# Kernel tuning notes

Hardware: AMD Instinct MI355X
Metric: run time of the kernel (lower is better)

## Reference

```python
import jax, jax.numpy as jnp
import numpy as np

B, S, D, H = 2, 2048, 1024, 16
HD = D // H  # 64


def setup_inputs() -> dict:
    key = jax.random.key(0)
    k1, k2, k3, k4, k5, k6 = jax.random.split(key, 6)
    x = jax.random.normal(k1, (B, S, D), dtype=jnp.float32)
    # binary mask source (1.0 = masked-out position), multiplied by -1e9 inside
    mask = (jax.random.uniform(k2, (B, S, S), dtype=jnp.float32) < 0.1).astype(jnp.float32)
    lim = 1.0 / np.sqrt(D)
    Wqkv = jax.random.uniform(k3, (D, 3 * D), dtype=jnp.float32, minval=-lim, maxval=lim)
    bqkv = jax.random.uniform(k4, (3 * D,), dtype=jnp.float32, minval=-lim, maxval=lim)
    Wo = jax.random.uniform(k5, (D, D), dtype=jnp.float32, minval=-lim, maxval=lim)
    bo = jax.random.uniform(k6, (D,), dtype=jnp.float32, minval=-lim, maxval=lim)
    return {"x": x, "mask": mask, "Wqkv": Wqkv, "bqkv": bqkv, "Wo": Wo, "bo": bo}


def reference(x, mask, Wqkv, bqkv, Wo, bo):
    b, s, d = x.shape
    qkv = x @ Wqkv + bqkv                              # [B,S,3D]
    qkv = qkv.reshape(b, s, 3, H, HD).transpose(2, 0, 3, 1, 4)  # [3,B,H,S,HD]
    q, k, v = qkv[0], qkv[1], qkv[2]
    scale = 1.0 / jnp.sqrt(jnp.float32(HD))
    scores = jnp.einsum('bhqd,bhkd->bhqk', q, k) * scale
    scores = scores + mask[:, None, :, :] * (-1e9)     # broadcast over heads
    attn = jax.nn.softmax(scores, axis=-1)             # [B,H,S,S]
    values = jnp.einsum('bhqk,bhkd->bhqd', attn, v)    # [B,H,S,HD]
    # faithful to source: permute(1,0,2,3) then reshape(B,S,H*HD)
    values = values.transpose(1, 0, 2, 3).reshape(b, s, H * HD)
    return values @ Wo + bo
```

## Files before the change

kernel.cpp:

```cpp
#include <hip/hip_runtime.h>
#include <stdint.h>

#define BB 2
#define SS 2048
#define DD 1024
#define HH 16
#define HD 64
#define BH 32
#define BS 4096

typedef short bf16x8 __attribute__((ext_vector_type(8)));
typedef float f32x4 __attribute__((ext_vector_type(4)));

static __device__ __forceinline__ unsigned short f2bf(float f) {
    union { float f; unsigned int u; } x;
    x.f = f;
    unsigned int u = x.u;
    unsigned int r = u + 0x7FFFu + ((u >> 16) & 1u);
    return (unsigned short)(r >> 16);
}

static __device__ __forceinline__ void gld16(unsigned short* lds, const unsigned short* g) {
    __builtin_amdgcn_global_load_lds(
        (const __attribute__((address_space(1))) unsigned int*)g,
        (__attribute__((address_space(3))) unsigned int*)lds,
        16, 0, 0);
}

__global__ __launch_bounds__(256) void prep(
    const float* __restrict__ x, unsigned short* __restrict__ xb,
    const float* __restrict__ Wqkv, unsigned short* __restrict__ WqkvT,
    const float* __restrict__ Wo, unsigned short* __restrict__ WoT,
    const float* __restrict__ mask, unsigned int* __restrict__ mbitsT,
    unsigned int* __restrict__ kmaxsq) {
    __shared__ float tile[32][33];
    int bid = blockIdx.x;
    int tid = threadIdx.x;
    if (bid < 4096) {
        int i = (bid * 256 + tid) * 4;
        float4 v = *(const float4*)(x + i);
        ushort4 o;
        o.x = f2bf(v.x); o.y = f2bf(v.y); o.z = f2bf(v.z); o.w = f2bf(v.w);
        *(ushort4*)(xb + i) = o;
    } else if (bid < 8192) {
        const float* W;
        unsigned short* WT;
        int N, t;
        if (bid < 7168) { W = Wqkv; WT = WqkvT; N = 3072; t = bid - 4096; }
        else            { W = Wo;   WT = WoT;   N = 1024; t = bid - 7168; }
        const int K = 1024;
        int nx = N >> 5;
        int n0 = (t % nx) * 32, k0 = (t / nx) * 32;
        int tx = tid & 31, ty = tid >> 5;
#pragma unroll
        for (int i = 0; i < 4; i++)
            tile[ty + i * 8][tx] = W[(size_t)(k0 + ty + i * 8) * N + n0 + tx];
        __syncthreads();
#pragma unroll
        for (int i = 0; i < 4; i++)
            WT[(size_t)(n0 + ty + i * 8) * K + k0 + tx] = f2bf(tile[tx][ty + i * 8]);
    } else if (bid == 8192) {
        if (tid < BH) kmaxsq[tid] = 0u;
    } else {
        size_t i = (size_t)(bid - 8193) * 256 + tid;
        float v = mask[i];
        unsigned long long bal = __ballot(v != 0.0f);
        int lane = tid & 63;
        int kw = (int)((i & 2047) >> 5);
        int sq = (int)((i >> 11) & 2047);
        int b = (int)(i >> 22);
        if (lane == 0)
            mbitsT[((size_t)b * 64 + kw) * 2048 + sq] = (unsigned int)bal;
        else if (lane == 32)
            mbitsT[((size_t)b * 64 + kw) * 2048 + sq] = (unsigned int)(bal >> 32);
    }
}

__global__ __launch_bounds__(256) void k_norm_max(
    const unsigned short* __restrict__ k_ws, unsigned int* __restrict__ kmaxsq) {
    int bh = blockIdx.x >> 3, part = blockIdx.x & 7;
    int row = part * 256 + threadIdx.x;
    const unsigned short* rp = k_ws + ((size_t)bh * 2048 + row) * 64;
    float ss = 0.f;
#pragma unroll
    for (int i = 0; i < 64; i += 8) {
        bf16x8 v;
        __builtin_memcpy(&v, rp + i, 16);
#pragma unroll
        for (int j = 0; j < 8; j++) {
            float f = __uint_as_float(((unsigned int)(unsigned short)v[j]) << 16);
            ss += f * f;
        }
    }
#pragma unroll
    for (int d = 1; d < 64; d <<= 1) ss = fmaxf(ss, __shfl_xor(ss, d, 64));
    if ((threadIdx.x & 63) == 0) atomicMax(kmaxsq + bh, __float_as_uint(ss));
}

__global__ __launch_bounds__(256) void qkv_gemm(
    const unsigned short* __restrict__ xb,
    const unsigned short* __restrict__ WqkvT,
    const float* __restrict__ bqkv,
    unsigned short* __restrict__ q_ws,
    unsigned short* __restrict__ k_ws,
    unsigned short* __restrict__ vB) {
    __shared__ unsigned short ldsA[4096], ldsB[4096];
    int gx = blockIdx.x;
    int tid = threadIdx.x;
    int m0 = (gx / 24) * 128, n0 = (gx % 24) * 128;
    int w = tid >> 6, lane = tid & 63, quad = lane >> 4, l15 = lane & 15;

    int r = tid >> 2, p = tid & 3;
    int c = (p - (r >> 1)) & 3;
    const unsigned short* gA0 = xb + (size_t)(m0 + r) * 1024 + c * 8;
    const unsigned short* gA1 = gA0 + (size_t)64 * 1024;
    const unsigned short* gB0 = WqkvT + (size_t)(n0 + r) * 1024 + c * 8;
    const unsigned short* gB1 = gB0 + (size_t)64 * 1024;
    unsigned short* lA0 = ldsA + w * 512;
    unsigned short* lA1 = ldsA + 2048 + w * 512;
    unsigned short* lB0 = ldsB + w * 512;
    unsigned short* lB1 = ldsB + 2048 + w * 512;

    int wm = w >> 1, wn = w & 1;
    int posq = ((quad + (l15 >> 1)) & 3) * 8;
    int aoff = (wm * 64 + l15) * 32 + posq;
    int boff = (wn * 64 + l15) * 32 + posq;

    f32x4 acc[4][4] = {};
    for (int k0 = 0; k0 < 1024; k0 += 32) {
        __syncthreads();
        gld16(lA0, gA0 + k0);
        gld16(lA1, gA1 + k0);
        gld16(lB0, gB0 + k0);
        gld16(lB1, gB1 + k0);
        __syncthreads();
        bf16x8 af[4], bfr[4];
#pragma unroll
        for (int i = 0; i < 4; i++) {
            af[i]  = *(const bf16x8*)(ldsA + aoff + i * 512);
            bfr[i] = *(const bf16x8*)(ldsB + boff + i * 512);
        }
#pragma unroll
        for (int i = 0; i < 4; i++)
#pragma unroll
            for (int j = 0; j < 4; j++)
                acc[i][j] = __builtin_amdgcn_mfma_f32_16x16x32_bf16(af[i], bfr[j], acc[i][j], 0, 0, 0);
    }

    int t = n0 >> 10;
    int ncol0 = n0 + wn * 64;
    int hh = (ncol0 >> 6) & 15;
    int Rb = m0 + wm * 64 + quad * 4;

    if (t == 2) {
        int rowbase = m0 + wm * 64;
        int b = rowbase >> 11;
        int kt = (rowbase >> 6) & 31;
        int bh = b * 16 + hh;
#pragma unroll
        for (int j = 0; j < 4; j++) {
            int hd = j * 16 + l15;
            float bias = bqkv[ncol0 + hd];
#pragma unroll
            for (int i = 0; i < 4; i++) {
                unsigned short* dst = vB +
                    (((((size_t)bh * 32 + kt) * 2 + (i >> 1)) * 4 + quad) * 64 + hd) * 8 + (i & 1) * 4;
                ushort4 pk;
                pk.x = f2bf(acc[i][j][0] + bias);
                pk.y = f2bf(acc[i][j][1] + bias);
                pk.z = f2bf(acc[i][j][2] + bias);
                pk.w = f2bf(acc[i][j][3] + bias);
                *(ushort4*)dst = pk;
            }
        }
    } else {
        unsigned short* dst = (t == 0) ? q_ws : k_ws;
#pragma unroll
        for (int j = 0; j < 4; j++) {
            int hd = j * 16 + l15;
            float bias = bqkv[ncol0 + hd];
#pragma unroll
            for (int i = 0; i < 4; i++) {
                int row = Rb + i * 16;
                int b = row >> 11, s = row & 2047;
                int bh = b * 16 + hh;
#pragma unroll
                for (int rr = 0; rr < 4; rr++)
                    dst[((size_t)(bh * 2048 + s + rr)) * 64 + hd] = f2bf(acc[i][j][rr] + bias);
            }
        }
    }
}

__global__ __launch_bounds__(256) void out_gemm(
    const unsigned short* __restrict__ Amat,
    const unsigned short* __restrict__ WoT,
    const float* __restrict__ bo,
    float* __restrict__ out) {
    __shared__ unsigned short ldsA[4096], ldsB[2048];
    int gx = blockIdx.x;
    int m0 = (gx / 16) * 128, n0 = (gx % 16) * 64;
    int tid = threadIdx.x;
    int w = tid >> 6, lane = tid & 63, quad = lane >> 4, l15 = lane & 15;

    int r = tid >> 2, p = tid & 3;
    int c = (p - (r >> 1)) & 3;
    const unsigned short* gA0 = Amat + (size_t)(m0 + r) * 1024 + c * 8;
    const unsigned short* gA1 = gA0 + (size_t)64 * 1024;
    const unsigned short* gB0 = WoT + (size_t)(n0 + r) * 1024 + c * 8;
    unsigned short* lA0 = ldsA + w * 512;
    unsigned short* lA1 = ldsA + 2048 + w * 512;
    unsigned short* lB0 = ldsB + w * 512;

    int wm = w >> 1, wn = w & 1;
    int posq = ((quad + (l15 >> 1)) & 3) * 8;
    int aoff = (wm * 64 + l15) * 32 + posq;
    int boff = (wn * 32 + l15) * 32 + posq;

    f32x4 acc[4][2] = {};
    for (int k0 = 0; k0 < 1024; k0 += 32) {
        __syncthreads();
        gld16(lA0, gA0 + k0);
        gld16(lA1, gA1 + k0);
        gld16(lB0, gB0 + k0);
        __syncthreads();
        bf16x8 af[4], bfr[2];
#pragma unroll
        for (int i = 0; i < 4; i++) af[i] = *(const bf16x8*)(ldsA + aoff + i * 512);
#pragma unroll
        for (int j = 0; j < 2; j++) bfr[j] = *(const bf16x8*)(ldsB + boff + j * 512);
#pragma unroll
        for (int i = 0; i < 4; i++)
#pragma unroll
            for (int j = 0; j < 2; j++)
                acc[i][j] = __builtin_amdgcn_mfma_f32_16x16x32_bf16(af[i], bfr[j], acc[i][j], 0, 0, 0);
    }
    int ncol0 = n0 + wn * 32;
    int Rb = m0 + wm * 64 + quad * 4;
#pragma unroll
    for (int j = 0; j < 2; j++) {
        int col = ncol0 + j * 16 + l15;
        float bias = bo[col];
#pragma unroll
        for (int i = 0; i < 4; i++) {
            int row = Rb + i * 16;
#pragma unroll
            for (int rr = 0; rr < 4; rr++)
                out[(size_t)(row + rr) * 1024 + col] = acc[i][j][rr] + bias;
        }
    }
}

__global__ __launch_bounds__(256) void attn(
    const unsigned short* __restrict__ q_ws,
    const unsigned short* __restrict__ k_ws,
    const unsigned short* __restrict__ vB,
    const unsigned int* __restrict__ mbitsT,
    const unsigned int* __restrict__ kmaxsq,
    unsigned short* __restrict__ o_ws) {
    __shared__ unsigned short ldsK[2][4096];
    __shared__ unsigned short ldsV[2][4096];

    int tid = threadIdx.x;
    int w = tid >> 6, lane = tid & 63, quad = lane >> 4, l15 = lane & 15;
    int bx = blockIdx.x;
    int bh = bx >> 5, qt = bx & 31;
    int b = bh >> 4, h = bh & 15;

    int q = qt * 64 + w * 16 + l15;
    const unsigned short* qptr = q_ws + ((size_t)(bh * 2048 + q)) * 64 + quad * 8;
    bf16x8 qf0 = *(const bf16x8*)(qptr);
    bf16x8 qf1 = *(const bf16x8*)(qptr + 32);

    float ss = 0.f;
#pragma unroll
    for (int j = 0; j < 8; j++) {
        float a = __uint_as_float(((unsigned int)(unsigned short)qf0[j]) << 16);
        float c = __uint_as_float(((unsigned int)(unsigned short)qf1[j]) << 16);
        ss += a * a + c * c;
    }
    ss += __shfl_xor(ss, 16, 64);
    ss += __shfl_xor(ss, 32, 64);
    const float c2 = 0.125f * 1.44269504089f;
    float Km = sqrtf(__uint_as_float(kmaxsq[bh]));
    float M = sqrtf(ss) * Km * c2 * 1.01f + 0.05f;
    const float Cs = c2 * 8388608.0f;
    float Ds = (127.0f - M) * 8388608.0f;

    const unsigned int* mb = mbitsT + (size_t)b * 64 * 2048 + q;
    const unsigned short* kbase = k_ws + (size_t)bh * 2048 * 64;
    const unsigned short* vbb = vB + (size_t)bh * 32 * 4096;

    int srow = (lane >> 3);
    int spos = lane & 7;
    int r0 = w * 16 + srow;
    int r1 = r0 + 8;
    int g0 = spos ^ (r0 & 7);
    int g1 = spos ^ (r1 & 7);
    unsigned short* dK0 = &ldsK[0][0] + w * 1024 + lane * 8;
    unsigned short* dV0 = &ldsV[0][0] + w * 1024 + lane * 8;

    f32x4 oacc[4] = {};
    f32x4 lacc = {};
    bf16x8 onesA;
#pragma unroll
    for (int j = 0; j < 8; j++) onesA[j] = (short)0x3F80;

    int sw = (l15 & 7);
    int q4 = quad * 4;

    {
        gld16(dK0, kbase + ((size_t)r0) * 64 + g0 * 8);
        gld16(dK0 + 512, kbase + ((size_t)r1) * 64 + g1 * 8);
        const unsigned short* vsrc = vbb + w * 1024 + lane * 8;
        gld16(dV0, vsrc);
        gld16(dV0 + 512, vsrc + 512);
    }

    for (int kt = 0; kt < 32; kt++) {
        int cur = kt & 1;
        __syncthreads();
        if (kt < 31) {
            int nb2 = (cur ^ 1) * 4096;
            size_t kb = (size_t)((kt + 1) * 64);
            gld16(dK0 + nb2, kbase + (kb + r0) * 64 + g0 * 8);
            gld16(dK0 + nb2 + 512, kbase + (kb + r1) * 64 + g1 * 8);
            const unsigned short* vsrc = vbb + (size_t)(kt + 1) * 4096 + w * 1024 + lane * 8;
            gld16(dV0 + nb2, vsrc);
            gld16(dV0 + nb2 + 512, vsrc + 512);
        }
        unsigned int w0 = mb[(size_t)(2 * kt) * 2048];
        unsigned int w1 = mb[(size_t)(2 * kt + 1) * 2048];

        const unsigned short* Kc = &ldsK[cur][0];
        const unsigned short* Vc = &ldsV[cur][0];
        f32x4 sacc[4];
#pragma unroll
        for (int nt = 0; nt < 4; nt++) {
            const unsigned short* kr = Kc + (nt * 16 + l15) * 64;
            bf16x8 kf0, kf1;
            __builtin_memcpy(&kf0, kr + (quad ^ sw) * 8, 16);
            __builtin_memcpy(&kf1, kr + ((quad + 4) ^ sw) * 8, 16);
            f32x4 z = {};
            z = __builtin_amdgcn_mfma_f32_16x16x32_bf16(kf0, qf0, z, 0, 0, 0);
            z = __builtin_amdgcn_mfma_f32_16x16x32_bf16(kf1, qf1, z, 0, 0, 0);
            sacc[nt] = z;
        }
        unsigned int s0 = w0 >> q4;
        unsigned int s1 = w1 >> q4;
        unsigned int dw[4][2];
#pragma unroll
        for (int nt = 0; nt < 4; nt++) {
            unsigned int sel = (nt & 2) ? s1 : s0;
            unsigned int u[4];
#pragma unroll
            for (int rr = 0; rr < 4; rr++) {
                float y = __builtin_fmaf(sacc[nt][rr], Cs, Ds);
                if ((sel >> ((nt & 1) * 16 + rr)) & 1u) y = 0.f;
                u[rr] = (unsigned int)(int)y;
            }
            dw[nt][0] = __builtin_amdgcn_perm(u[1], u[0], 0x07060302u);
            dw[nt][1] = __builtin_amdgcn_perm(u[3], u[2], 0x07060302u);
        }
#pragma unroll
        for (int ks2 = 0; ks2 < 2; ks2++) {
            union { bf16x8 v; unsigned int d[4]; } bfr;
            bfr.d[0] = dw[2 * ks2][0];
            bfr.d[1] = dw[2 * ks2][1];
            bfr.d[2] = dw[2 * ks2 + 1][0];
            bfr.d[3] = dw[2 * ks2 + 1][1];
#pragma unroll
            for (int nb = 0; nb < 4; nb++) {
                bf16x8 vf;
                __builtin_memcpy(&vf, Vc + ((ks2 * 4 + quad) * 64 + nb * 16 + l15) * 8, 16);
                oacc[nb] = __builtin_amdgcn_mfma_f32_16x16x32_bf16(vf, bfr.v, oacc[nb], 0, 0, 0);
            }
            lacc = __builtin_amdgcn_mfma_f32_16x16x32_bf16(onesA, bfr.v, lacc, 0, 0, 0);
        }
    }

    float linv = 1.0f / lacc[0];
    unsigned short* base = o_ws + ((size_t)((h * 2 + b) * 2048 + q)) * 64;
#pragma unroll
    for (int nb = 0; nb < 4; nb++) {
        ushort4 pk;
        pk.x = f2bf(oacc[nb][0] * linv);
        pk.y = f2bf(oacc[nb][1] * linv);
        pk.z = f2bf(oacc[nb][2] * linv);
        pk.w = f2bf(oacc[nb][3] * linv);
        *(ushort4*)(base + nb * 16 + quad * 4) = pk;
    }
}


extern "C" void kernel_launch(void* const* d_in, const int* in_sizes, int n_in,
                              void* d_out, int out_size, void* d_ws, size_t ws_size,
                              hipStream_t stream) {
    const float* x    = (const float*)d_in[0];
    const float* mask = (const float*)d_in[1];
    const float* Wqkv = (const float*)d_in[2];
    const float* bqkv = (const float*)d_in[3];
    const float* Wo   = (const float*)d_in[4];
    const float* bo   = (const float*)d_in[5];
    float* out = (float*)d_out;

    char* ws = (char*)d_ws;
    unsigned short* xb    = (unsigned short*)(ws);
    unsigned short* WqkvT = (unsigned short*)(ws + ((size_t)8 << 20));
    unsigned short* WoT   = (unsigned short*)(ws + ((size_t)14 << 20));
    unsigned short* q_ws  = (unsigned short*)(ws + ((size_t)16 << 20));
    unsigned short* k_ws  = (unsigned short*)(ws + ((size_t)24 << 20));
    unsigned short* vB    = (unsigned short*)(ws + ((size_t)32 << 20));
    unsigned short* o_ws  = (unsigned short*)(ws + ((size_t)40 << 20));
    unsigned int*   mbits = (unsigned int*)(ws + ((size_t)48 << 20));
    unsigned int*   kmaxsq = (unsigned int*)(ws + ((size_t)49 << 20));

    prep<<<8193 + 32768, 256, 0, stream>>>(x, xb, Wqkv, WqkvT, Wo, WoT, mask, mbits, kmaxsq);
    qkv_gemm<<<768, 256, 0, stream>>>(xb, WqkvT, bqkv, q_ws, k_ws, vB);
    k_norm_max<<<BH * 8, 256, 0, stream>>>(k_ws, kmaxsq);
    attn<<<1024, 256, 0, stream>>>(q_ws, k_ws, vB, mbits, kmaxsq, o_ws);
    out_gemm<<<512, 256, 0, stream>>>(o_ws, WoT, bo, out);
}
```

Before: 247.1 us.

## Split attention waves over query and key halves, load K/V directly to registers

```diff
diff --git a/kernel.cpp b/kernel.cpp
--- a/kernel.cpp
+++ b/kernel.cpp
@@ -251,144 +251,168 @@
     }
 }
 
-__global__ __launch_bounds__(256) void attn(
+__global__ __launch_bounds__(256, 4) void attn(
     const unsigned short* __restrict__ q_ws,
     const unsigned short* __restrict__ k_ws,
     const unsigned short* __restrict__ vB,
     const unsigned int* __restrict__ mbitsT,
     const unsigned int* __restrict__ kmaxsq,
     unsigned short* __restrict__ o_ws) {
-    __shared__ unsigned short ldsK[2][4096];
-    __shared__ unsigned short ldsV[2][4096];
+    __shared__ float ocomb[2][64][33];
+    __shared__ float lcomb[2][32];
 
     int tid = threadIdx.x;
     int w = tid >> 6, lane = tid & 63, quad = lane >> 4, l15 = lane & 15;
+    int wq = w & 1, wk = w >> 1;
     int bx = blockIdx.x;
     int bh = bx >> 5, qt = bx & 31;
     int b = bh >> 4, h = bh & 15;
-
-    int q = qt * 64 + w * 16 + l15;
-    const unsigned short* qptr = q_ws + ((size_t)(bh * 2048 + q)) * 64 + quad * 8;
-    bf16x8 qf0 = *(const bf16x8*)(qptr);
-    bf16x8 qf1 = *(const bf16x8*)(qptr + 32);
-
-    float ss = 0.f;
-#pragma unroll
-    for (int j = 0; j < 8; j++) {
-        float a = __uint_as_float(((unsigned int)(unsigned short)qf0[j]) << 16);
-        float c = __uint_as_float(((unsigned int)(unsigned short)qf1[j]) << 16);
-        ss += a * a + c * c;
-    }
-    ss += __shfl_xor(ss, 16, 64);
-    ss += __shfl_xor(ss, 32, 64);
+    int qtb = qt * 64;
+
+    bf16x8 qf[2][2];
+#pragma unroll
+    for (int nt = 0; nt < 2; nt++) {
+        const unsigned short* qp =
+            q_ws + ((size_t)(bh * 2048 + qtb + wq * 32 + nt * 16 + l15)) * 64 + quad * 8;
+        qf[nt][0] = *(const bf16x8*)(qp);
+        qf[nt][1] = *(const bf16x8*)(qp + 32);
+    }
+
+    float ssn[2];
+#pragma unroll
+    for (int nt = 0; nt < 2; nt++) {
+        float ss = 0.f;
+#pragma unroll
+        for (int ks = 0; ks < 2; ks++)
+#pragma unroll
+            for (int j = 0; j < 8; j++) {
+                float a = __uint_as_float(((unsigned int)(unsigned short)qf[nt][ks][j]) << 16);
+                ss += a * a;
+            }
+        ss += __shfl_xor(ss, 16, 64);
+        ss += __shfl_xor(ss, 32, 64);
+        ssn[nt] = ss;
+    }
     const float c2 = 0.125f * 1.44269504089f;
     float Km = sqrtf(__uint_as_float(kmaxsq[bh]));
-    float M = sqrtf(ss) * Km * c2 * 1.01f + 0.05f;
     const float Cs = c2 * 8388608.0f;
-    float Ds = (127.0f - M) * 8388608.0f;
-
-    const unsigned int* mb = mbitsT + (size_t)b * 64 * 2048 + q;
-    const unsigned short* kbase = k_ws + (size_t)bh * 2048 * 64;
-    const unsigned short* vbb = vB + (size_t)bh * 32 * 4096;
-
-    int srow = (lane >> 3);
-    int spos = lane & 7;
-    int r0 = w * 16 + srow;
-    int r1 = r0 + 8;
-    int g0 = spos ^ (r0 & 7);
-    int g1 = spos ^ (r1 & 7);
-    unsigned short* dK0 = &ldsK[0][0] + w * 1024 + lane * 8;
-    unsigned short* dV0 = &ldsV[0][0] + w * 1024 + lane * 8;
-
-    f32x4 oacc[4] = {};
-    f32x4 lacc = {};
+    float Ds[2];
+#pragma unroll
+    for (int nt = 0; nt < 2; nt++) {
+        float M = sqrtf(ssn[nt]) * Km * c2 * 1.01f + 0.05f;
+        Ds[nt] = (127.0f - M) * 8388608.0f;
+    }
+
+    const unsigned short* kbase = k_ws + (size_t)bh * 2048 * 64
+                                  + (size_t)(wk * 32 + l15) * 64 + quad * 8;
+    const unsigned short* vbase = vB + (size_t)bh * 32 * 4096
+                                  + (size_t)(wk * 4 + quad) * 512 + l15 * 8;
+    const unsigned int* mbq = mbitsT + (size_t)b * 64 * 2048 + qtb + wq * 32 + l15;
+
+    f32x4 oacc[4][2] = {};
+    f32x4 lacc[2] = {};
     bf16x8 onesA;
 #pragma unroll
     for (int j = 0; j < 8; j++) onesA[j] = (short)0x3F80;
 
-    int sw = (l15 & 7);
     int q4 = quad * 4;
 
-    {
-        gld16(dK0, kbase + ((size_t)r0) * 64 + g0 * 8);
-        gld16(dK0 + 512, kbase + ((size_t)r1) * 64 + g1 * 8);
-        const unsigned short* vsrc = vbb + w * 1024 + lane * 8;
-        gld16(dV0, vsrc);
-        gld16(dV0 + 512, vsrc + 512);
-    }
-
+    bf16x8 kf[2][2][2];
+    unsigned int mw[2][2];
+#pragma unroll
+    for (int mg = 0; mg < 2; mg++) {
+        kf[0][mg][0] = *(const bf16x8*)(kbase + mg * 1024);
+        kf[0][mg][1] = *(const bf16x8*)(kbase + mg * 1024 + 32);
+    }
+    mw[0][0] = mbq[(size_t)wk * 2048];
+    mw[0][1] = mbq[(size_t)wk * 2048 + 16];
+
+#pragma unroll 2
     for (int kt = 0; kt < 32; kt++) {
-        int cur = kt & 1;
-        __syncthreads();
+        int par = kt & 1, nxt = par ^ 1;
         if (kt < 31) {
-            int nb2 = (cur ^ 1) * 4096;
-            size_t kb = (size_t)((kt + 1) * 64);
-            gld16(dK0 + nb2, kbase + (kb + r0) * 64 + g0 * 8);
-            gld16(dK0 + nb2 + 512, kbase + (kb + r1) * 64 + g1 * 8);
-            const unsigned short* vsrc = vbb + (size_t)(kt + 1) * 4096 + w * 1024 + lane * 8;
-            gld16(dV0 + nb2, vsrc);
-            gld16(dV0 + nb2 + 512, vsrc + 512);
-        }
-        unsigned int w0 = mb[(size_t)(2 * kt) * 2048];
-        unsigned int w1 = mb[(size_t)(2 * kt + 1) * 2048];
-
-        const unsigned short* Kc = &ldsK[cur][0];
-        const unsigned short* Vc = &ldsV[cur][0];
-        f32x4 sacc[4];
-#pragma unroll
-        for (int nt = 0; nt < 4; nt++) {
-            const unsigned short* kr = Kc + (nt * 16 + l15) * 64;
-            bf16x8 kf0, kf1;
-            __builtin_memcpy(&kf0, kr + (quad ^ sw) * 8, 16);
-            __builtin_memcpy(&kf1, kr + ((quad + 4) ^ sw) * 8, 16);
-            f32x4 z = {};
-            z = __builtin_amdgcn_mfma_f32_16x16x32_bf16(kf0, qf0, z, 0, 0, 0);
-            z = __builtin_amdgcn_mfma_f32_16x16x32_bf16(kf1, qf1, z, 0, 0, 0);
-            sacc[nt] = z;
-        }
-        unsigned int s0 = w0 >> q4;
-        unsigned int s1 = w1 >> q4;
-        unsigned int dw[4][2];
-#pragma unroll
-        for (int nt = 0; nt < 4; nt++) {
-            unsigned int sel = (nt & 2) ? s1 : s0;
-            unsigned int u[4];
-#pragma unroll
-            for (int rr = 0; rr < 4; rr++) {
-                float y = __builtin_fmaf(sacc[nt][rr], Cs, Ds);
-                if ((sel >> ((nt & 1) * 16 + rr)) & 1u) y = 0.f;
-                u[rr] = (unsigned int)(int)y;
-            }
-            dw[nt][0] = __builtin_amdgcn_perm(u[1], u[0], 0x07060302u);
-            dw[nt][1] = __builtin_amdgcn_perm(u[3], u[2], 0x07060302u);
-        }
-#pragma unroll
-        for (int ks2 = 0; ks2 < 2; ks2++) {
+            const unsigned short* kp = kbase + (size_t)(kt + 1) * 4096;
+#pragma unroll
+            for (int mg = 0; mg < 2; mg++) {
+                kf[nxt][mg][0] = *(const bf16x8*)(kp + mg * 1024);
+                kf[nxt][mg][1] = *(const bf16x8*)(kp + mg * 1024 + 32);
+            }
+            mw[nxt][0] = mbq[(size_t)((kt + 1) * 2 + wk) * 2048];
+            mw[nxt][1] = mbq[(size_t)((kt + 1) * 2 + wk) * 2048 + 16];
+        }
+        bf16x8 vf[4];
+        {
+            const unsigned short* vp = vbase + (size_t)kt * 4096;
+#pragma unroll
+            for (int hdg = 0; hdg < 4; hdg++)
+                vf[hdg] = *(const bf16x8*)(vp + hdg * 128);
+        }
+        f32x4 sacc[2][2];
+#pragma unroll
+        for (int mg = 0; mg < 2; mg++)
+#pragma unroll
+            for (int nt = 0; nt < 2; nt++) {
+                f32x4 z = {};
+                z = __builtin_amdgcn_mfma_f32_16x16x32_bf16(kf[par][mg][0], qf[nt][0], z, 0, 0, 0);
+                z = __builtin_amdgcn_mfma_f32_16x16x32_bf16(kf[par][mg][1], qf[nt][1], z, 0, 0, 0);
+                sacc[mg][nt] = z;
+            }
+#pragma unroll
+        for (int nt = 0; nt < 2; nt++) {
+            unsigned int sel = mw[par][nt] >> q4;
             union { bf16x8 v; unsigned int d[4]; } bfr;
-            bfr.d[0] = dw[2 * ks2][0];
-            bfr.d[1] = dw[2 * ks2][1];
-            bfr.d[2] = dw[2 * ks2 + 1][0];
-            bfr.d[3] = dw[2 * ks2 + 1][1];
-#pragma unroll
-            for (int nb = 0; nb < 4; nb++) {
-                bf16x8 vf;
-                __builtin_memcpy(&vf, Vc + ((ks2 * 4 + quad) * 64 + nb * 16 + l15) * 8, 16);
-                oacc[nb] = __builtin_amdgcn_mfma_f32_16x16x32_bf16(vf, bfr.v, oacc[nb], 0, 0, 0);
-            }
-            lacc = __builtin_amdgcn_mfma_f32_16x16x32_bf16(onesA, bfr.v, lacc, 0, 0, 0);
-        }
-    }
-
-    float linv = 1.0f / lacc[0];
-    unsigned short* base = o_ws + ((size_t)((h * 2 + b) * 2048 + q)) * 64;
-#pragma unroll
-    for (int nb = 0; nb < 4; nb++) {
-        ushort4 pk;
-        pk.x = f2bf(oacc[nb][0] * linv);
-        pk.y = f2bf(oacc[nb][1] * linv);
-        pk.z = f2bf(oacc[nb][2] * linv);
-        pk.w = f2bf(oacc[nb][3] * linv);
-        *(ushort4*)(base + nb * 16 + quad * 4) = pk;
+#pragma unroll
+            for (int mg = 0; mg < 2; mg++) {
+                unsigned int u[4];
+#pragma unroll
+                for (int rr = 0; rr < 4; rr++) {
+                    float y = __builtin_fmaf(sacc[mg][nt][rr], Cs, Ds[nt]);
+                    if ((sel >> (mg * 16 + rr)) & 1u) y = 0.f;
+                    u[rr] = (unsigned int)(int)y;
+                }
+                bfr.d[mg * 2 + 0] = __builtin_amdgcn_perm(u[1], u[0], 0x07060302u);
+                bfr.d[mg * 2 + 1] = __builtin_amdgcn_perm(u[3], u[2], 0x07060302u);
+            }
+#pragma unroll
+            for (int hdg = 0; hdg < 4; hdg++)
+                oacc[hdg][nt] = __builtin_amdgcn_mfma_f32_16x16x32_bf16(vf[hdg], bfr.v, oacc[hdg][nt], 0, 0, 0);
+            lacc[nt] = __builtin_amdgcn_mfma_f32_16x16x32_bf16(onesA, bfr.v, lacc[nt], 0, 0, 0);
+        }
+    }
+
+    if (wk == 1) {
+#pragma unroll
+        for (int hdg = 0; hdg < 4; hdg++)
+#pragma unroll
+            for (int nt = 0; nt < 2; nt++)
+#pragma unroll
+                for (int rr = 0; rr < 4; rr++)
+                    ocomb[wq][hdg * 16 + quad * 4 + rr][nt * 16 + l15] = oacc[hdg][nt][rr];
+        if (quad == 0) {
+            lcomb[wq][l15] = lacc[0][0];
+            lcomb[wq][16 + l15] = lacc[1][0];
+        }
+    }
+    __syncthreads();
+    if (wk == 0) {
+        float linv[2];
+#pragma unroll
+        for (int nt = 0; nt < 2; nt++)
+            linv[nt] = 1.0f / (lacc[nt][0] + lcomb[wq][nt * 16 + l15]);
+#pragma unroll
+        for (int nt = 0; nt < 2; nt++) {
+            int q = qtb + wq * 32 + nt * 16 + l15;
+            unsigned short* base = o_ws + ((size_t)((h * 2 + b) * 2048 + q)) * 64;
+#pragma unroll
+            for (int hdg = 0; hdg < 4; hdg++) {
+                ushort4 pk;
+                pk.x = f2bf((oacc[hdg][nt][0] + ocomb[wq][hdg * 16 + quad * 4 + 0][nt * 16 + l15]) * linv[nt]);
+                pk.y = f2bf((oacc[hdg][nt][1] + ocomb[wq][hdg * 16 + quad * 4 + 1][nt * 16 + l15]) * linv[nt]);
+                pk.z = f2bf((oacc[hdg][nt][2] + ocomb[wq][hdg * 16 + quad * 4 + 2][nt * 16 + l15]) * linv[nt]);
+                pk.w = f2bf((oacc[hdg][nt][3] + ocomb[wq][hdg * 16 + quad * 4 + 3][nt * 16 + l15]) * linv[nt]);
+                *(ushort4*)(base + hdg * 16 + quad * 4) = pk;
+            }
+        }
     }
 }
 
```

Measured after the change: 268.5 us. 8.6% more time.
